# Kernel tuning notes

Measured on AMD Instinct MI355X. Metric: run time of the kernel, lower is better.

Reference implementation:

```python
import jax, jax.numpy as jnp
import numpy as np

B, W, C_BLK, N_EMBD, N_HEADS = 512, 128, 24, 32, 2


def setup_inputs() -> dict:
    key = jax.random.key(0)
    k1, k2, k3, k4 = jax.random.split(key, 4)
    x = jax.random.normal(k1, (B, W, C_BLK, N_EMBD), dtype=jnp.float32)
    x_end_idx = jax.random.randint(k2, (B, W), 0, C_BLK, dtype=jnp.int32)
    # nn.Linear(n_embd, 3*n_embd, bias=False): store transposed so y = x @ w
    w_attn = jax.random.normal(k3, (N_EMBD, 3 * N_EMBD), dtype=jnp.float32) * (1.0 / np.sqrt(N_EMBD))
    w_proj = jax.random.normal(k4, (N_EMBD, N_EMBD), dtype=jnp.float32) * (1.0 / np.sqrt(N_EMBD))
    return {"x": x, "x_end_idx": x_end_idx, "w_attn": w_attn, "w_proj": w_proj}


def reference(x, x_end_idx, w_attn, w_proj):
    # x: [B, W, c, C]; causal self-attention over the char axis c, per (batch, word).
    Bd, Wd, c, C = x.shape
    H = N_HEADS
    D = C // H
    qkv = x @ w_attn                               # [B, W, c, 3C]
    q, k, v = jnp.split(qkv, 3, axis=-1)
    # [B, W, H, c, D]
    q = q.reshape(Bd, Wd, c, H, D).transpose(0, 1, 3, 2, 4)
    k = k.reshape(Bd, Wd, c, H, D).transpose(0, 1, 3, 2, 4)
    v = v.reshape(Bd, Wd, c, H, D).transpose(0, 1, 3, 2, 4)
    scale = 1.0 / jnp.sqrt(jnp.asarray(D, dtype=x.dtype))
    scores = jnp.einsum('bwhqd,bwhkd->bwhqk', q, k) * scale   # [B, W, H, c, c]
    causal = jnp.tril(jnp.ones((c, c), dtype=bool))
    scores = jnp.where(causal, scores, jnp.asarray(-jnp.inf, dtype=scores.dtype))
    att = jax.nn.softmax(scores, axis=-1)
    out = jnp.einsum('bwhqk,bwhkd->bwhqd', att, v)            # [B, W, H, c, D]
    out = out.transpose(0, 1, 3, 2, 4).reshape(Bd, Wd, c, C)
    out = out @ w_proj                                        # c_proj (dropout in eval mode = identity)
    out = x + out                                             # residual
    # Vectorized last-token gather: pick out[b, w, x_end_idx[b, w], :]
    idx = x_end_idx[:, :, None, None].astype(jnp.int32)       # [B, W, 1, 1]
    samples = jnp.take_along_axis(out, jnp.broadcast_to(idx, (Bd, Wd, 1, C)), axis=2)
    return samples.squeeze(2)                                 # [B, W, C]
```

## Files before the change

### kernel.cpp

```cpp
#include <hip/hip_runtime.h>


#define CB      24
#define CC      32
#define DD      16
#define THREEC  96
#define NBW     (512 * 128)
#define WPB     4
#define XSS     34

struct __align__(16) WaveSmem {
    float xs[CB][XSS];
    float rks[2][CC];
    float ps[2][CC];
    float ys[2][CC];
    float os[CC];
    float pad[2];
};

__device__ __forceinline__ void wave_fence() {
    __asm__ volatile("s_waitcnt lgkmcnt(0)" ::: "memory");
}

__global__ __launch_bounds__(256, 8) void char_attn_kernel(
    const float* __restrict__ x,
    const int*   __restrict__ xend,
    const float* __restrict__ w_attn,
    const float* __restrict__ w_proj,
    float*       __restrict__ out)
{
    __shared__ WaveSmem sm[WPB];

    const int tid  = threadIdx.x;
    const int lane = tid & 63;
    const int wave = tid >> 6;
    WaveSmem& S = sm[wave];

    const int bid  = blockIdx.x * WPB + wave;
    const int i32  = lane & 31;
    const int half = lane >> 5;

    const int qidx = xend[bid];
    const int L    = qidx + 1;
    const float* xb = x + (size_t)bid * (CB * CC);

    {
        const float2* xb2 = (const float2*)xb;
        const int n2 = L * (CC / 2);
        for (int t = lane; t < n2; t += 64) {
            float2 v = xb2[t];
            const int r = t >> 4, c = (t & 15) * 2;
            *(float2*)&S.xs[r][c] = v;
        }
    }
    wave_fence();

    float qv;
    {
        const int cb = half * DD;
        float a0 = 0.f, a1 = 0.f;
        #pragma unroll
        for (int t = 0; t < DD; t += 2) {
            a0 = fmaf(S.xs[qidx][cb + t],     w_attn[(cb + t) * THREEC + i32],     a0);
            a1 = fmaf(S.xs[qidx][cb + t + 1], w_attn[(cb + t + 1) * THREEC + i32], a1);
        }
        qv = a0 + a1;
        qv += __shfl_xor(qv, 32);
    }

    {
        const float4* w4 = (const float4*)&w_attn[i32 * THREEC + CC + DD * half];
        float4 w0 = w4[0], w1 = w4[1], w2 = w4[2], w3 = w4[3];
        const int db = DD * half;
        float a0 = 0.f, a1 = 0.f;
        a0 = fmaf(w0.x, __shfl(qv, db + 0),  a0); a1 = fmaf(w0.y, __shfl(qv, db + 1),  a1);
        a0 = fmaf(w0.z, __shfl(qv, db + 2),  a0); a1 = fmaf(w0.w, __shfl(qv, db + 3),  a1);
        a0 = fmaf(w1.x, __shfl(qv, db + 4),  a0); a1 = fmaf(w1.y, __shfl(qv, db + 5),  a1);
        a0 = fmaf(w1.z, __shfl(qv, db + 6),  a0); a1 = fmaf(w1.w, __shfl(qv, db + 7),  a1);
        a0 = fmaf(w2.x, __shfl(qv, db + 8),  a0); a1 = fmaf(w2.y, __shfl(qv, db + 9),  a1);
        a0 = fmaf(w2.z, __shfl(qv, db + 10), a0); a1 = fmaf(w2.w, __shfl(qv, db + 11), a1);
        a0 = fmaf(w3.x, __shfl(qv, db + 12), a0); a1 = fmaf(w3.y, __shfl(qv, db + 13), a1);
        a0 = fmaf(w3.z, __shfl(qv, db + 14), a0); a1 = fmaf(w3.w, __shfl(qv, db + 15), a1);
        S.rks[half][i32] = (a0 + a1) * 0.25f;
    }
    wave_fence();

    {
        float sc = -INFINITY;
        if (i32 <= qidx) {
            float a0 = 0.f, a1 = 0.f;
            #pragma unroll
            for (int c = 0; c < CC; c += 2) {
                a0 = fmaf(S.xs[i32][c],     S.rks[half][c],     a0);
                a1 = fmaf(S.xs[i32][c + 1], S.rks[half][c + 1], a1);
            }
            sc = a0 + a1;
        }
        float m = sc;
        #pragma unroll
        for (int off = 16; off >= 1; off >>= 1)
            m = fmaxf(m, __shfl_xor(m, off));
        const float e = (i32 <= qidx) ? __expf(sc - m) : 0.f;
        float sum = e;
        #pragma unroll
        for (int off = 16; off >= 1; off >>= 1)
            sum += __shfl_xor(sum, off);
        S.ps[half][i32] = e / sum;
    }
    wave_fence();

    {
        float acc = 0.f;
        for (int j = 0; j < L; ++j)
            acc = fmaf(S.ps[half][j], S.xs[j][i32], acc);
        S.ys[half][i32] = acc;
    }
    wave_fence();

    {
        const int hi = i32 >> 4;
        const int cb = half * DD;
        float a0 = 0.f, a1 = 0.f;
        #pragma unroll
        for (int t = 0; t < DD; t += 2) {
            a0 = fmaf(S.ys[hi][cb + t],     w_attn[(cb + t) * THREEC + 2 * CC + i32],     a0);
            a1 = fmaf(S.ys[hi][cb + t + 1], w_attn[(cb + t + 1) * THREEC + 2 * CC + i32], a1);
        }
        float t = a0 + a1;
        t += __shfl_xor(t, 32);
        if (lane < CC) S.os[i32] = t;
    }
    wave_fence();

    {
        const int cb = half * DD;
        float a0 = 0.f, a1 = 0.f;
        #pragma unroll
        for (int t = 0; t < DD; t += 2) {
            a0 = fmaf(S.os[cb + t],     w_proj[(cb + t) * CC + i32],     a0);
            a1 = fmaf(S.os[cb + t + 1], w_proj[(cb + t + 1) * CC + i32], a1);
        }
        float t = a0 + a1;
        t += __shfl_xor(t, 32);
        if (lane < CC)
            out[(size_t)bid * CC + i32] = t + S.xs[qidx][i32];
    }
}

extern "C" void kernel_launch(void* const* d_in, const int* in_sizes, int n_in,
                              void* d_out, int out_size, void* d_ws, size_t ws_size,
                              hipStream_t stream) {
    const float* x      = (const float*)d_in[0];
    const int*   xend   = (const int*)d_in[1];
    const float* w_attn = (const float*)d_in[2];
    const float* w_proj = (const float*)d_in[3];
    float* out = (float*)d_out;

    char_attn_kernel<<<dim3(NBW / WPB), dim3(WPB * 64), 0, stream>>>(
        x, xend, w_attn, w_proj, out);
}
```

Before: 303.4 us.

## Precompute fused Wq·Wk and Wv·Wproj matrices per head in prologue kernel

Adds a small kernel, run on every launch, that folds the query-key weight product (with the scale) and the value-projection product into two per-head 32x32 matrices in device globals. The main kernel then needs one matvec for the key-side vector and one for the output instead of chained matvecs with shuffles and an extra LDS stage. It also loads the x tile with a fixed unrolled count, zero-filling the padding rows, and runs the P·V loop over all 24 rows with float2 LDS reads. The cost is an extra kernel launch and serialization before the main kernel, plus wasted work on masked rows.

```diff
diff --git a/kernel.cpp b/kernel.cpp
--- a/kernel.cpp
+++ b/kernel.cpp
@@ -9,13 +9,30 @@
 #define WPB     4
 #define XSS     34
 
+__device__ __align__(16) float g_Mt[2][CC][CC];
+__device__ __align__(16) float g_Pt[2][CC][CC];
+
+__global__ void precompute_mp(const float* __restrict__ w_attn,
+                              const float* __restrict__ w_proj)
+{
+    const int idx = blockIdx.x * 256 + threadIdx.x;
+    const int h = idx >> 10, c = (idx >> 5) & 31, e = idx & 31;
+    float m = 0.f, p = 0.f;
+    #pragma unroll
+    for (int d = 0; d < DD; ++d) {
+        const int i = DD * h + d;
+        m = fmaf(w_attn[e * THREEC + i],          w_attn[c * THREEC + CC + i], m);
+        p = fmaf(w_attn[e * THREEC + 2 * CC + i], w_proj[i * CC + c],          p);
+    }
+    g_Mt[h][c][e] = 0.25f * m;
+    g_Pt[h][c][e] = p;
+}
+
 struct __align__(16) WaveSmem {
     float xs[CB][XSS];
     float rks[2][CC];
     float ps[2][CC];
     float ys[2][CC];
-    float os[CC];
-    float pad[2];
 };
 
 __device__ __forceinline__ void wave_fence() {
@@ -25,8 +42,6 @@
 __global__ __launch_bounds__(256, 8) void char_attn_kernel(
     const float* __restrict__ x,
     const int*   __restrict__ xend,
-    const float* __restrict__ w_attn,
-    const float* __restrict__ w_proj,
     float*       __restrict__ out)
 {
     __shared__ WaveSmem sm[WPB];
@@ -47,41 +62,31 @@
     {
         const float2* xb2 = (const float2*)xb;
         const int n2 = L * (CC / 2);
-        for (int t = lane; t < n2; t += 64) {
-            float2 v = xb2[t];
+        #pragma unroll
+        for (int t0 = 0; t0 < CB * (CC / 2); t0 += 64) {
+            const int t = t0 + lane;
+            float2 v = make_float2(0.f, 0.f);
+            if (t < n2) v = xb2[t];
             const int r = t >> 4, c = (t & 15) * 2;
             *(float2*)&S.xs[r][c] = v;
         }
     }
     wave_fence();
 
-    float qv;
     {
-        const int cb = half * DD;
-        float a0 = 0.f, a1 = 0.f;
+        const float4* m4 = (const float4*)&g_Mt[half][i32][0];
+        float a0 = 0.f, a1 = 0.f, a2 = 0.f, a3 = 0.f;
         #pragma unroll
-        for (int t = 0; t < DD; t += 2) {
-            a0 = fmaf(S.xs[qidx][cb + t],     w_attn[(cb + t) * THREEC + i32],     a0);
-            a1 = fmaf(S.xs[qidx][cb + t + 1], w_attn[(cb + t + 1) * THREEC + i32], a1);
+        for (int e4 = 0; e4 < 8; ++e4) {
+            const float4 mv = m4[e4];
+            const float2 x0 = *(const float2*)&S.xs[qidx][e4 * 4];
+            const float2 x1 = *(const float2*)&S.xs[qidx][e4 * 4 + 2];
+            a0 = fmaf(mv.x, x0.x, a0);
+            a1 = fmaf(mv.y, x0.y, a1);
+            a2 = fmaf(mv.z, x1.x, a2);
+            a3 = fmaf(mv.w, x1.y, a3);
         }
-        qv = a0 + a1;
-        qv += __shfl_xor(qv, 32);
-    }
-
-    {
-        const float4* w4 = (const float4*)&w_attn[i32 * THREEC + CC + DD * half];
-        float4 w0 = w4[0], w1 = w4[1], w2 = w4[2], w3 = w4[3];
-        const int db = DD * half;
-        float a0 = 0.f, a1 = 0.f;
-        a0 = fmaf(w0.x, __shfl(qv, db + 0),  a0); a1 = fmaf(w0.y, __shfl(qv, db + 1),  a1);
-        a0 = fmaf(w0.z, __shfl(qv, db + 2),  a0); a1 = fmaf(w0.w, __shfl(qv, db + 3),  a1);
-        a0 = fmaf(w1.x, __shfl(qv, db + 4),  a0); a1 = fmaf(w1.y, __shfl(qv, db + 5),  a1);
-        a0 = fmaf(w1.z, __shfl(qv, db + 6),  a0); a1 = fmaf(w1.w, __shfl(qv, db + 7),  a1);
-        a0 = fmaf(w2.x, __shfl(qv, db + 8),  a0); a1 = fmaf(w2.y, __shfl(qv, db + 9),  a1);
-        a0 = fmaf(w2.z, __shfl(qv, db + 10), a0); a1 = fmaf(w2.w, __shfl(qv, db + 11), a1);
-        a0 = fmaf(w3.x, __shfl(qv, db + 12), a0); a1 = fmaf(w3.y, __shfl(qv, db + 13), a1);
-        a0 = fmaf(w3.z, __shfl(qv, db + 14), a0); a1 = fmaf(w3.w, __shfl(qv, db + 15), a1);
-        S.rks[half][i32] = (a0 + a1) * 0.25f;
+        S.rks[half][i32] = (a0 + a1) + (a2 + a3);
     }
     wave_fence();
 
@@ -91,8 +96,10 @@
             float a0 = 0.f, a1 = 0.f;
             #pragma unroll
             for (int c = 0; c < CC; c += 2) {
-                a0 = fmaf(S.xs[i32][c],     S.rks[half][c],     a0);
-                a1 = fmaf(S.xs[i32][c + 1], S.rks[half][c + 1], a1);
+                const float2 xv = *(const float2*)&S.xs[i32][c];
+                const float2 rv = *(const float2*)&S.rks[half][c];
+                a0 = fmaf(xv.x, rv.x, a0);
+                a1 = fmaf(xv.y, rv.y, a1);
             }
             sc = a0 + a1;
         }
@@ -105,42 +112,36 @@
         #pragma unroll
         for (int off = 16; off >= 1; off >>= 1)
             sum += __shfl_xor(sum, off);
-        S.ps[half][i32] = e / sum;
+        S.ps[half][i32] = __fdividef(e, sum);
     }
     wave_fence();
 
     {
-        float acc = 0.f;
-        for (int j = 0; j < L; ++j)
-            acc = fmaf(S.ps[half][j], S.xs[j][i32], acc);
-        S.ys[half][i32] = acc;
+        float a0 = 0.f, a1 = 0.f;
+        #pragma unroll
+        for (int j = 0; j < CB; j += 2) {
+            const float2 p2 = *(const float2*)&S.ps[half][j];
+            a0 = fmaf(p2.x, S.xs[j][i32],     a0);
+            a1 = fmaf(p2.y, S.xs[j + 1][i32], a1);
+        }
+        S.ys[half][i32] = a0 + a1;
     }
     wave_fence();
 
     {
-        const int hi = i32 >> 4;
-        const int cb = half * DD;
-        float a0 = 0.f, a1 = 0.f;
+        const float4* p4 = (const float4*)&g_Pt[half][i32][0];
+        float a0 = 0.f, a1 = 0.f, a2 = 0.f, a3 = 0.f;
         #pragma unroll
-        for (int t = 0; t < DD; t += 2) {
-            a0 = fmaf(S.ys[hi][cb + t],     w_attn[(cb + t) * THREEC + 2 * CC + i32],     a0);
-            a1 = fmaf(S.ys[hi][cb + t + 1], w_attn[(cb + t + 1) * THREEC + 2 * CC + i32], a1);
+        for (int e4 = 0; e4 < 8; ++e4) {
+            const float4 pv = p4[e4];
+            const float2 y0 = *(const float2*)&S.ys[half][e4 * 4];
+            const float2 y1 = *(const float2*)&S.ys[half][e4 * 4 + 2];
+            a0 = fmaf(pv.x, y0.x, a0);
+            a1 = fmaf(pv.y, y0.y, a1);
+            a2 = fmaf(pv.z, y1.x, a2);
+            a3 = fmaf(pv.w, y1.y, a3);
         }
-        float t = a0 + a1;
-        t += __shfl_xor(t, 32);
-        if (lane < CC) S.os[i32] = t;
-    }
-    wave_fence();
-
-    {
-        const int cb = half * DD;
-        float a0 = 0.f, a1 = 0.f;
-        #pragma unroll
-        for (int t = 0; t < DD; t += 2) {
-            a0 = fmaf(S.os[cb + t],     w_proj[(cb + t) * CC + i32],     a0);
-            a1 = fmaf(S.os[cb + t + 1], w_proj[(cb + t + 1) * CC + i32], a1);
-        }
-        float t = a0 + a1;
+        float t = (a0 + a1) + (a2 + a3);
         t += __shfl_xor(t, 32);
         if (lane < CC)
             out[(size_t)bid * CC + i32] = t + S.xs[qidx][i32];
@@ -156,6 +157,7 @@
     const float* w_proj = (const float*)d_in[3];
     float* out = (float*)d_out;
 
+    precompute_mp<<<dim3(8), dim3(256), 0, stream>>>(w_attn, w_proj);
     char_attn_kernel<<<dim3(NBW / WPB), dim3(WPB * 64), 0, stream>>>(
-        x, xend, w_attn, w_proj, out);
+        x, xend, out);
 }
```

After: 346.3 us. +14.1%, slower.
